# Optimization experiments

Measured on AMD Instinct MI355X. Metric: run time of the kernel, lower is better.

The kernel has to match this reference:

```python
import jax, jax.numpy as jnp
import numpy as np

B, S, D, H = 2, 2048, 1024, 16
DK = D // H  # 64


def setup_inputs() -> dict:
    key = jax.random.key(0)
    k0, k1, k2, k3, k4, k5, k6 = jax.random.split(key, 7)
    scale = 0.02
    return {
        "q": jax.random.normal(k0, (B, S, D), dtype=jnp.float32),
        "k": jax.random.normal(k1, (B, S, D), dtype=jnp.float32),
        "v": jax.random.normal(k2, (B, S, D), dtype=jnp.float32),
        # per-head Q/K projection weights (n_head separate Linear layers, bias=False)
        "Wq": jax.random.normal(k3, (H, D, DK), dtype=jnp.float32) * scale,
        "Wk": jax.random.normal(k4, (H, D, DK), dtype=jnp.float32) * scale,
        # shared V projection (the same v_layer object is reused for every head)
        "Wv": jax.random.normal(k5, (D, DK), dtype=jnp.float32) * scale,
        # output projection fc: d_v -> d_model, bias=False
        "Wo": jax.random.normal(k6, (DK, D), dtype=jnp.float32) * scale,
    }


def reference(q, k, v, Wq, Wk, Wv, Wo):
    d_k = Wq.shape[-1]
    # batched per-head projections (replaces the Python loop over heads)
    qs = jnp.einsum("bsd,hdk->bhsk", q, Wq)          # [B,H,S,DK]
    ks = jnp.einsum("bsd,hdk->bhsk", k, Wk)          # [B,H,S,DK]
    vs = jnp.einsum("bsd,dk->bsk", v, Wv)            # [B,S,DK] shared across heads
    scores = jnp.einsum("bhsk,bhtk->bhst", qs, ks) / jnp.sqrt(
        jnp.asarray(d_k, dtype=jnp.float32)
    )                                                 # [B,H,S,S]
    attn = jax.nn.softmax(scores, axis=-1)            # [B,H,S,S]; dropout = identity (eval)
    heads = jnp.einsum("bhst,btk->bhsk", attn, vs)    # [B,H,S,DK]
    head = heads.mean(axis=1)                         # mean over heads, not concat
    attn_mean = attn.mean(axis=1)                     # [B,S,S]
    out = jnp.einsum("bsk,kd->bsd", head, Wo)         # [B,S,D]; dropout = identity
    return (out, attn_mean)
```

## Files before the change

kernel.cpp:

```cpp
#include <hip/hip_runtime.h>

#define B_ 2
#define S_ 2048
#define D_ 1024
#define H_ 16
#define DK_ 64

typedef __bf16 bf8 __attribute__((ext_vector_type(8)));
typedef float f4 __attribute__((ext_vector_type(4)));
typedef unsigned short u16x8 __attribute__((ext_vector_type(8)));

__device__ __forceinline__ unsigned short f2bf_bits(float f) {
  unsigned int u = __float_as_uint(f);
  return (unsigned short)((u + 0x7fffu + ((u >> 16) & 1u)) >> 16);
}

__device__ __forceinline__ bf8 pack_bf8(f4 lo, f4 hi) {
  u16x8 u;
  u[0] = f2bf_bits(lo[0]); u[1] = f2bf_bits(lo[1]);
  u[2] = f2bf_bits(lo[2]); u[3] = f2bf_bits(lo[3]);
  u[4] = f2bf_bits(hi[0]); u[5] = f2bf_bits(hi[1]);
  u[6] = f2bf_bits(hi[2]); u[7] = f2bf_bits(hi[3]);
  union { u16x8 u; bf8 b; } x; x.u = u; return x.b;
}

__device__ __forceinline__ bf8 ldb(const unsigned short* p) {
  return *reinterpret_cast<const bf8*>(p);
}

__device__ __forceinline__ void stage16(const void* g, void* l) {
  __builtin_amdgcn_global_load_lds(
      (const __attribute__((address_space(1))) void*)g,
      (__attribute__((address_space(3))) void*)l, 16, 0, 0);
}

#define MFMA(a, b, c) __builtin_amdgcn_mfma_f32_16x16x32_bf16((a), (b), (c), 0, 0, 0)

__global__ void k_prep(const float* __restrict__ q, const float* __restrict__ k,
                       const float* __restrict__ wq, const float* __restrict__ wk,
                       const float* __restrict__ wv, const float* __restrict__ wo,
                       unsigned short* __restrict__ qb, unsigned short* __restrict__ kb,
                       unsigned short* __restrict__ wqt, unsigned short* __restrict__ wkt,
                       unsigned short* __restrict__ wvt, unsigned short* __restrict__ wot) {
  __shared__ float tl[64 * 65];
  int bid = blockIdx.x, tid = threadIdx.x;
  const int rr = tid >> 6, cc = tid & 63;
  if (bid < 4096) {
    int which = bid >> 11;
    long i = ((long)(bid & 2047) * 256 + tid) * 8;
    const float* src = which ? k : q;
    unsigned short* dst = which ? kb : qb;
    f4 lo = *reinterpret_cast<const f4*>(src + i);
    f4 hi = *reinterpret_cast<const f4*>(src + i + 4);
    *reinterpret_cast<bf8*>(dst + i) = pack_bf8(lo, hi);
  } else if (bid < 4352) {
    int blk = bid - 4096;
    int h = blk >> 4, d0 = (blk & 15) * 64;
    for (int m = 0; m < 2; ++m) {
      const float* src = m ? wk : wq;
      unsigned short* dst = m ? wkt : wqt;
      if (m) __syncthreads();
#pragma unroll
      for (int it = 0; it < 16; ++it) {
        int d = it * 4 + rr;
        tl[cc * 65 + d] = src[(long)h * 65536 + (d0 + d) * 64 + cc];
      }
      __syncthreads();
#pragma unroll
      for (int it = 0; it < 16; ++it) {
        int n = it * 4 + rr;
        dst[(long)h * 65536 + n * 1024 + d0 + cc] = f2bf_bits(tl[n * 65 + cc]);
      }
    }
  } else if (bid < 4368) {
    int d0 = (bid - 4352) * 64;
#pragma unroll
    for (int it = 0; it < 16; ++it) {
      int d = it * 4 + rr;
      tl[cc * 65 + d] = wv[(long)(d0 + d) * 64 + cc];
    }
    __syncthreads();
#pragma unroll
    for (int it = 0; it < 16; ++it) {
      int n = it * 4 + rr;
      wvt[(long)n * 1024 + d0 + cc] = f2bf_bits(tl[n * 65 + cc]);
    }
  } else {
    int d0 = (bid - 4368) * 64;
#pragma unroll
    for (int it = 0; it < 16; ++it) {
      int kk = it * 4 + rr;
      tl[cc * 65 + kk] = wo[(long)kk * 1024 + d0 + cc];
    }
    __syncthreads();
#pragma unroll
    for (int it = 0; it < 16; ++it) {
      int ddl = it * 4 + rr;
      wot[(long)(d0 + ddl) * 64 + cc] = f2bf_bits(tl[ddl * 65 + cc]);
    }
  }
}

__global__ __launch_bounds__(256) void k_gemm_qk(
    const unsigned short* __restrict__ qb, const unsigned short* __restrict__ kb,
    const unsigned short* __restrict__ wqt, const unsigned short* __restrict__ wkt,
    unsigned short* __restrict__ qsb, unsigned short* __restrict__ ksb) {
  __shared__ unsigned short lds[8192];
  const int tid = threadIdx.x, wave = tid >> 6, lane = tid & 63;
  const int l15 = lane & 15, quad = lane >> 4;
  const int m0 = blockIdx.x * 128, n0 = blockIdx.y * 128;
  const int which = blockIdx.z;
  const unsigned short* A = which ? kb : qb;
  const unsigned short* W = which ? wkt : wqt;
  unsigned short* C = which ? ksb : qsb;
  const float scale = which ? 1.0f : 0.18033688011112042f;
  const int wr = wave >> 1, wc = wave & 1;

  f4 acc[4][4];
#pragma unroll
  for (int i = 0; i < 4; ++i)
#pragma unroll
    for (int j = 0; j < 4; ++j) acc[i][j] = f4{0.f, 0.f, 0.f, 0.f};

  const int sl15 = tid & 15, squad = (tid >> 4) & 3, st = tid >> 6;
  const unsigned short* gA = A + (long)(m0 + st * 16 + sl15) * D_ + squad * 8;
  const unsigned short* gB = W + (long)(n0 + st * 16 + sl15) * D_ + squad * 8;

  for (int k0 = 0; k0 < D_; k0 += 32) {
    stage16(gA + k0, lds + tid * 8);
    stage16(gA + 64 * D_ + k0, lds + 2048 + tid * 8);
    stage16(gB + k0, lds + 4096 + tid * 8);
    stage16(gB + 64 * D_ + k0, lds + 6144 + tid * 8);
    __syncthreads();
    bf8 aF[4], bF[4];
#pragma unroll
    for (int mi = 0; mi < 4; ++mi)
      aF[mi] = ldb(lds + (wr * 4 + mi) * 512 + lane * 8);
#pragma unroll
    for (int ni = 0; ni < 4; ++ni)
      bF[ni] = ldb(lds + 4096 + (wc * 4 + ni) * 512 + lane * 8);
#pragma unroll
    for (int mi = 0; mi < 4; ++mi)
#pragma unroll
      for (int ni = 0; ni < 4; ++ni)
        acc[mi][ni] = MFMA(aF[mi], bF[ni], acc[mi][ni]);
    __syncthreads();
  }
#pragma unroll
  for (int mi = 0; mi < 4; ++mi)
#pragma unroll
    for (int r = 0; r < 4; ++r) {
      long row = m0 + wr * 64 + mi * 16 + quad * 4 + r;
#pragma unroll
      for (int ni = 0; ni < 4; ++ni)
        C[row * D_ + n0 + wc * 64 + ni * 16 + l15] = f2bf_bits(acc[mi][ni][r] * scale);
    }
}

__global__ __launch_bounds__(256) void k_pv(
    const float* __restrict__ v, const unsigned short* __restrict__ wvt,
    float* __restrict__ pv) {
  const int tid = threadIdx.x, wave = tid >> 6, lane = tid & 63;
  const int l15 = lane & 15, quad = lane >> 4;
  const int rg = blockIdx.x, kc = blockIdx.y;
  const int row0 = rg * 64 + wave * 16;
  const float* arow = v + (long)(row0 + l15) * D_ + kc * 256 + quad * 8;
  const unsigned short* wbase = wvt + kc * 256 + quad * 8;
  f4 acc[4];
  for (int i = 0; i < 4; ++i) acc[i] = f4{0.f, 0.f, 0.f, 0.f};
  for (int k0 = 0; k0 < 256; k0 += 32) {
    f4 alo = *reinterpret_cast<const f4*>(arow + k0);
    f4 ahi = *reinterpret_cast<const f4*>(arow + k0 + 4);
    bf8 a = pack_bf8(alo, ahi);
#pragma unroll
    for (int i = 0; i < 4; ++i) {
      bf8 bf = ldb(wbase + (long)(i * 16 + l15) * D_ + k0);
      acc[i] = MFMA(a, bf, acc[i]);
    }
  }
#pragma unroll
  for (int i = 0; i < 4; ++i)
#pragma unroll
    for (int r = 0; r < 4; ++r)
      pv[((long)kc * 4096 + row0 + quad * 4 + r) * 64 + i * 16 + l15] = acc[i][r];
}

__global__ void k_vred(const float* __restrict__ pv, unsigned short* __restrict__ vst) {
  int e = blockIdx.x * 256 + threadIdx.x;
  int t = e & 2047, dk = (e >> 11) & 63, b = e >> 17;
  long row = (long)b * S_ + t;
  float s = pv[row * 64 + dk] + pv[(4096 + row) * 64 + dk] +
            pv[(8192 + row) * 64 + dk] + pv[(12288 + row) * 64 + dk];
  vst[e] = f2bf_bits(s);
}

__global__ __launch_bounds__(512) void k_denom(
    const unsigned short* __restrict__ qsb, const unsigned short* __restrict__ ksb,
    float* __restrict__ recip) {
  __shared__ unsigned short lds[16384];
  const int tid = threadIdx.x, wave = tid >> 6, lane = tid & 63;
  const int l15 = lane & 15, quad = lane >> 4;
  const int n = blockIdx.x, xcd = n & 7, slot = n >> 3;
  const int b = xcd >> 2;
  const int h = ((xcd & 3) << 2) | (slot & 3);
  const int stile = slot >> 2;
  const int s0 = stile * 128 + wave * 16;

  const unsigned short* qrow = qsb + ((long)(b * S_) + s0 + l15) * D_ + h * 64 + quad * 8;
  bf8 a0 = ldb(qrow);
  bf8 a1 = ldb(qrow + 32);

  const int sl15 = tid & 15, squad = (tid >> 4) & 3, stt = (tid >> 6) & 7;
  const unsigned short* g0 =
      ksb + ((long)(b * S_) + stt * 16 + sl15) * D_ + h * 64 + squad * 8;

  stage16(g0, lds + tid * 8);
  stage16(g0 + 32, lds + 4096 + tid * 8);
  asm volatile("s_waitcnt vmcnt(0)" ::: "memory");
  __builtin_amdgcn_s_barrier();
  int cur = 0;

  f4 sum = f4{0.f, 0.f, 0.f, 0.f};
  for (int it = 0; it < 16; ++it) {
    if (it + 1 < 16) {
      const unsigned short* gn = g0 + (long)(it + 1) * 128 * D_;
      unsigned short* nb = lds + (cur ^ 1) * 8192;
      stage16(gn, nb + tid * 8);
      stage16(gn + 32, nb + 4096 + tid * 8);
    }
    const unsigned short* base = lds + cur * 8192;
    __builtin_amdgcn_s_setprio(1);
#pragma unroll
    for (int tt = 0; tt < 8; ++tt) {
      bf8 b0 = ldb(base + tt * 512 + lane * 8);
      bf8 b1 = ldb(base + 4096 + tt * 512 + lane * 8);
      f4 d = f4{0.f, 0.f, 0.f, 0.f};
      d = MFMA(a0, b0, d);
      d = MFMA(a1, b1, d);
#pragma unroll
      for (int r = 0; r < 4; ++r) sum[r] += __builtin_amdgcn_exp2f(d[r]);
    }
    __builtin_amdgcn_s_setprio(0);
    if (it + 1 < 16) {
      asm volatile("s_waitcnt vmcnt(0)" ::: "memory");
      __builtin_amdgcn_s_barrier();
      cur ^= 1;
    }
  }
#pragma unroll
  for (int m = 1; m < 16; m <<= 1) {
#pragma unroll
    for (int r = 0; r < 4; ++r) sum[r] += __shfl_xor(sum[r], m, 64);
  }
  if (l15 == 0) {
    float* rp = recip + (long)(b * H_ + h) * S_ + s0 + quad * 4;
#pragma unroll
    for (int r = 0; r < 4; ++r) rp[r] = 1.0f / (16.0f * sum[r]);
  }
}

__global__ __launch_bounds__(512) void k_attn(
    const unsigned short* __restrict__ qsb, const unsigned short* __restrict__ ksb,
    const float* __restrict__ recip, float* __restrict__ am) {
  __shared__ unsigned short lds[16384];
  const int tid = threadIdx.x, wave = tid >> 6, lane = tid & 63;
  const int l15 = lane & 15, quad = lane >> 4;
  const int n = blockIdx.x, xcd = n & 7, slot = n >> 3;
  const int b = xcd >> 2;
  const int tchunk = ((xcd & 1) << 3) | (slot & 7);
  const int stile = (((xcd >> 1) & 1) << 3) | (slot >> 3);
  const int s0 = stile * 128 + wave * 16;
  const int t0c = tchunk * 128;

  f4 acc[8];
#pragma unroll
  for (int tt = 0; tt < 8; ++tt) acc[tt] = f4{0.f, 0.f, 0.f, 0.f};

  const unsigned short* qbase = qsb + ((long)(b * S_) + s0 + l15) * D_ + quad * 8;
  const int sl15 = tid & 15, squad = (tid >> 4) & 3, stt = (tid >> 6) & 7;
  const unsigned short* g0 =
      ksb + ((long)(b * S_) + t0c + stt * 16 + sl15) * D_ + squad * 8;
  const float* rbase = recip + (long)(b * H_) * S_ + s0 + quad * 4;

  stage16(g0, lds + tid * 8);
  stage16(g0 + 32, lds + 4096 + tid * 8);
  bf8 a0 = ldb(qbase);
  bf8 a1 = ldb(qbase + 32);
  f4 rp = *reinterpret_cast<const f4*>(rbase);
  asm volatile("s_waitcnt vmcnt(0)" ::: "memory");
  __builtin_amdgcn_s_barrier();
  int cur = 0;

  for (int h = 0; h < H_; ++h) {
    bf8 a0n, a1n;
    f4 rpn;
    if (h + 1 < H_) {
      a0n = ldb(qbase + (h + 1) * 64);
      a1n = ldb(qbase + (h + 1) * 64 + 32);
      rpn = *reinterpret_cast<const f4*>(rbase + (long)(h + 1) * S_);
      __builtin_amdgcn_sched_barrier(0);
      const unsigned short* gn = g0 + (h + 1) * 64;
      unsigned short* nb = lds + (cur ^ 1) * 8192;
      stage16(gn, nb + tid * 8);
      stage16(gn + 32, nb + 4096 + tid * 8);
    }
    const unsigned short* base = lds + cur * 8192;
    __builtin_amdgcn_s_setprio(1);
#pragma unroll
    for (int tt = 0; tt < 8; ++tt) {
      bf8 b0 = ldb(base + tt * 512 + lane * 8);
      bf8 b1 = ldb(base + 4096 + tt * 512 + lane * 8);
      f4 d = f4{0.f, 0.f, 0.f, 0.f};
      d = MFMA(a0, b0, d);
      d = MFMA(a1, b1, d);
#pragma unroll
      for (int r = 0; r < 4; ++r) acc[tt][r] += rp[r] * __builtin_amdgcn_exp2f(d[r]);
    }
    __builtin_amdgcn_s_setprio(0);
    if (h + 1 < H_) {
      asm volatile("s_waitcnt vmcnt(0)" ::: "memory");
      __builtin_amdgcn_s_barrier();
      cur ^= 1;
      a0 = a0n;
      a1 = a1n;
      rp = rpn;
    }
  }
  float* obase = am + ((long)b * S_ + s0 + quad * 4) * S_ + t0c + l15;
#pragma unroll
  for (int tt = 0; tt < 8; ++tt)
#pragma unroll
    for (int r = 0; r < 4; ++r) obase[(long)r * S_ + tt * 16] = acc[tt][r];
}

__global__ __launch_bounds__(256) void k_hpart(
    const float* __restrict__ am, const unsigned short* __restrict__ vst,
    float* __restrict__ ph) {
  const int tid = threadIdx.x, wave = tid >> 6, lane = tid & 63;
  const int l15 = lane & 15, quad = lane >> 4;
  const int rg = blockIdx.x, kc = blockIdx.y;
  const int row0 = rg * 64 + wave * 16;
  const int b = row0 >> 11;
  const float* arow = am + (long)(row0 + l15) * S_ + kc * 512 + quad * 8;
  const unsigned short* vb = vst + (long)b * DK_ * S_ + kc * 512 + quad * 8;
  f4 acc[4];
  for (int i = 0; i < 4; ++i) acc[i] = f4{0.f, 0.f, 0.f, 0.f};
  for (int t0 = 0; t0 < 512; t0 += 32) {
    f4 alo = *reinterpret_cast<const f4*>(arow + t0);
    f4 ahi = *reinterpret_cast<const f4*>(arow + t0 + 4);
    bf8 a = pack_bf8(alo, ahi);
#pragma unroll
    for (int i = 0; i < 4; ++i) {
      bf8 bf = ldb(vb + (long)(i * 16 + l15) * S_ + t0);
      acc[i] = MFMA(a, bf, acc[i]);
    }
  }
#pragma unroll
  for (int i = 0; i < 4; ++i)
#pragma unroll
    for (int r = 0; r < 4; ++r)
      ph[((long)kc * 4096 + row0 + quad * 4 + r) * 64 + i * 16 + l15] = acc[i][r];
}

__global__ void k_hred(const float* __restrict__ ph, unsigned short* __restrict__ headb) {
  int e = blockIdx.x * 256 + threadIdx.x;
  float s = ph[e] + ph[e + 4096 * 64] + ph[e + 2 * 4096 * 64] + ph[e + 3 * 4096 * 64];
  headb[e] = f2bf_bits(s);
}

__global__ __launch_bounds__(256) void k_out(
    const unsigned short* __restrict__ head, const unsigned short* __restrict__ wot,
    float* __restrict__ out) {
  const int tid = threadIdx.x, wave = tid >> 6, lane = tid & 63;
  const int l15 = lane & 15, quad = lane >> 4;
  const int dchunk = blockIdx.x, stile = blockIdx.y, b = blockIdx.z;
  const int s0 = stile * 64 + wave * 16;
  const int n0 = dchunk * 128;
  const unsigned short* hrow = head + ((long)b * S_ + s0 + l15) * DK_ + quad * 8;
  bf8 a0 = ldb(hrow);
  bf8 a1 = ldb(hrow + 32);
  const unsigned short* wb = wot + quad * 8;
  float* obase = out + ((long)b * S_ + s0 + quad * 4) * D_ + n0 + l15;
#pragma unroll
  for (int i = 0; i < 8; ++i) {
    const unsigned short* wp = wb + (long)(n0 + i * 16 + l15) * DK_;
    bf8 b0 = ldb(wp);
    bf8 b1 = ldb(wp + 32);
    f4 d = f4{0.f, 0.f, 0.f, 0.f};
    d = MFMA(a0, b0, d);
    d = MFMA(a1, b1, d);
#pragma unroll
    for (int r = 0; r < 4; ++r) obase[(long)r * D_ + i * 16] = d[r];
  }
}

extern "C" void kernel_launch(void* const* d_in, const int* in_sizes, int n_in,
                              void* d_out, int out_size, void* d_ws, size_t ws_size,
                              hipStream_t stream) {
  const float* q  = (const float*)d_in[0];
  const float* k  = (const float*)d_in[1];
  const float* v  = (const float*)d_in[2];
  const float* Wq = (const float*)d_in[3];
  const float* Wk = (const float*)d_in[4];
  const float* Wv = (const float*)d_in[5];
  const float* Wo = (const float*)d_in[6];

  float* out = (float*)d_out;
  float* am  = out + (long)B_ * S_ * D_;

  unsigned short* qsb  = (unsigned short*)d_ws;
  unsigned short* ksb  = qsb + 4194304;
  unsigned short* wqt  = ksb + 4194304;
  unsigned short* wkt  = wqt + 1048576;
  unsigned short* wvt  = wkt + 1048576;
  unsigned short* wot  = wvt + 65536;
  unsigned short* vst  = wot + 65536;
  unsigned short* headb= vst + 262144;
  float* recip = (float*)(headb + 262144);

  unsigned short* qb = (unsigned short*)am;
  unsigned short* kb = qb + 4194304;
  float* part = out;

  k_prep<<<4384, 256, 0, stream>>>(q, k, Wq, Wk, Wv, Wo, qb, kb, wqt, wkt, wvt, wot);
  k_gemm_qk<<<dim3(32, 8, 2), 256, 0, stream>>>(qb, kb, wqt, wkt, qsb, ksb);
  k_pv<<<dim3(64, 4), 256, 0, stream>>>(v, wvt, part);
  k_vred<<<1024, 256, 0, stream>>>(part, vst);
  k_denom<<<512, 512, 0, stream>>>(qsb, ksb, recip);
  k_attn<<<512, 512, 0, stream>>>(qsb, ksb, recip, am);
  k_hpart<<<dim3(64, 4), 256, 0, stream>>>(am, vst, part);
  k_hred<<<1024, 256, 0, stream>>>(part, headb);
  k_out<<<dim3(8, 32, 2), 256, 0, stream>>>(headb, wot, out);
}
```

Measured before the change: 240.0 us.

## Triple-buffer QK projection GEMM with async staging and XCD-aware block mapping

The Q/K projection GEMM gets a three-stage LDS ring buffer. Global-to-LDS loads for the tile two steps ahead are issued before the MFMAs run, and partial vmcnt waits plus raw barriers replace the two __syncthreads per K step. The grid is flattened to 1D and remapped so that blocks on the same XCD share the Q-vs-K choice and neighbouring row tiles, which is meant to improve L2 reuse. s_setprio is raised around the MFMA section. The cost is triple the LDS use, which may lower occupancy, and correctness now depends on stage16 being an async load counted by vmcnt.

```diff
diff --git a/kernel.cpp b/kernel.cpp
--- a/kernel.cpp
+++ b/kernel.cpp
@@ -105,11 +105,13 @@
     const unsigned short* __restrict__ qb, const unsigned short* __restrict__ kb,
     const unsigned short* __restrict__ wqt, const unsigned short* __restrict__ wkt,
     unsigned short* __restrict__ qsb, unsigned short* __restrict__ ksb) {
-  __shared__ unsigned short lds[8192];
-  const int tid = threadIdx.x, wave = tid >> 6, lane = tid & 63;
-  const int l15 = lane & 15, quad = lane >> 4;
-  const int m0 = blockIdx.x * 128, n0 = blockIdx.y * 128;
-  const int which = blockIdx.z;
+  __shared__ unsigned short lds[24576];
+  const int tid = threadIdx.x, wave = tid >> 6, lane = tid & 63;
+  const int l15 = lane & 15, quad = lane >> 4;
+  const int n = blockIdx.x, xcd = n & 7, slot = n >> 3;
+  const int which = xcd >> 2;
+  const int m0 = (((xcd & 3) << 3) | (slot & 7)) * 128;
+  const int n0 = (slot >> 3) * 128;
   const unsigned short* A = which ? kb : qb;
   const unsigned short* W = which ? wkt : wqt;
   unsigned short* C = which ? ksb : qsb;
@@ -126,25 +128,51 @@
   const unsigned short* gA = A + (long)(m0 + st * 16 + sl15) * D_ + squad * 8;
   const unsigned short* gB = W + (long)(n0 + st * 16 + sl15) * D_ + squad * 8;
 
-  for (int k0 = 0; k0 < D_; k0 += 32) {
-    stage16(gA + k0, lds + tid * 8);
-    stage16(gA + 64 * D_ + k0, lds + 2048 + tid * 8);
-    stage16(gB + k0, lds + 4096 + tid * 8);
-    stage16(gB + 64 * D_ + k0, lds + 6144 + tid * 8);
-    __syncthreads();
+  stage16(gA, lds + tid * 8);
+  stage16(gA + 64 * D_, lds + 2048 + tid * 8);
+  stage16(gB, lds + 4096 + tid * 8);
+  stage16(gB + 64 * D_, lds + 6144 + tid * 8);
+  stage16(gA + 32, lds + 8192 + tid * 8);
+  stage16(gA + 64 * D_ + 32, lds + 10240 + tid * 8);
+  stage16(gB + 32, lds + 12288 + tid * 8);
+  stage16(gB + 64 * D_ + 32, lds + 14336 + tid * 8);
+  asm volatile("s_waitcnt vmcnt(4)" ::: "memory");
+  __builtin_amdgcn_s_barrier();
+  int rd = 0;
+
+  for (int it = 0; it < 32; ++it) {
+    if (it + 2 < 32) {
+      const int k2 = (it + 2) * 32;
+      int wb = rd + 2; if (wb >= 3) wb -= 3;
+      unsigned short* nb = lds + wb * 8192;
+      stage16(gA + k2, nb + tid * 8);
+      stage16(gA + 64 * D_ + k2, nb + 2048 + tid * 8);
+      stage16(gB + k2, nb + 4096 + tid * 8);
+      stage16(gB + 64 * D_ + k2, nb + 6144 + tid * 8);
+    }
+    const unsigned short* base = lds + rd * 8192;
+    __builtin_amdgcn_s_setprio(1);
     bf8 aF[4], bF[4];
 #pragma unroll
     for (int mi = 0; mi < 4; ++mi)
-      aF[mi] = ldb(lds + (wr * 4 + mi) * 512 + lane * 8);
+      aF[mi] = ldb(base + (wr * 4 + mi) * 512 + lane * 8);
 #pragma unroll
     for (int ni = 0; ni < 4; ++ni)
-      bF[ni] = ldb(lds + 4096 + (wc * 4 + ni) * 512 + lane * 8);
+      bF[ni] = ldb(base + 4096 + (wc * 4 + ni) * 512 + lane * 8);
 #pragma unroll
     for (int mi = 0; mi < 4; ++mi)
 #pragma unroll
       for (int ni = 0; ni < 4; ++ni)
         acc[mi][ni] = MFMA(aF[mi], bF[ni], acc[mi][ni]);
-    __syncthreads();
+    __builtin_amdgcn_s_setprio(0);
+    if (it + 1 < 32) {
+      if (it + 2 < 32)
+        asm volatile("s_waitcnt vmcnt(4)" ::: "memory");
+      else
+        asm volatile("s_waitcnt vmcnt(0)" ::: "memory");
+      __builtin_amdgcn_s_barrier();
+      rd = (rd + 1 == 3) ? 0 : rd + 1;
+    }
   }
 #pragma unroll
   for (int mi = 0; mi < 4; ++mi)
@@ -423,7 +451,7 @@
   float* part = out;
 
   k_prep<<<4384, 256, 0, stream>>>(q, k, Wq, Wk, Wv, Wo, qb, kb, wqt, wkt, wvt, wot);
-  k_gemm_qk<<<dim3(32, 8, 2), 256, 0, stream>>>(qb, kb, wqt, wkt, qsb, ksb);
+  k_gemm_qk<<<512, 256, 0, stream>>>(qb, kb, wqt, wkt, qsb, ksb);
   k_pv<<<dim3(64, 4), 256, 0, stream>>>(v, wvt, part);
   k_vred<<<1024, 256, 0, stream>>>(part, vst);
   k_denom<<<512, 512, 0, stream>>>(qsb, ksb, recip);
```

New measurement: 237.2 us. About the same (-1.2%).
